# Kernel tuning notes

Hardware: AMD Instinct MI355X
Metric: run time of the kernel (lower is better)

Reference implementation:

```python
import jax, jax.numpy as jnp
import numpy as np

V, E, H, L, S, T = 100000, 256, 512, 50000, 512, 64


def setup_inputs() -> dict:
    key = jax.random.key(0)
    ks = jax.random.split(key, 14)
    s = 0.02
    return {
        "encoder_outputs": jax.random.normal(ks[0], (1, S, H), jnp.float32),
        "enc_h0": jax.random.normal(ks[1], (1, 1, H), jnp.float32),
        "enc_c0": jax.random.normal(ks[2], (1, 1, H), jnp.float32),
        "emb_table": jax.random.normal(ks[3], (V, E), jnp.float32) * s,
        "W_attn": jax.random.normal(ks[4], (H, E), jnp.float32) * s,
        "b_attn": jnp.zeros((H,), jnp.float32),
        "W_ih": jax.random.normal(ks[5], (4 * H, H), jnp.float32) * s,
        "W_hh": jax.random.normal(ks[6], (4 * H, H), jnp.float32) * s,
        "b_ih": jnp.zeros((4 * H,), jnp.float32),
        "b_hh": jnp.zeros((4 * H,), jnp.float32),
        "W_out": jax.random.normal(ks[7], (L, H), jnp.float32) * s,
        "b_out": jnp.zeros((L,), jnp.float32),
        "word_inputs": jax.random.randint(ks[8], (T,), 0, V),
        "labels": jax.random.randint(ks[9], (T,), 0, L),
    }


def reference(encoder_outputs, enc_h0, enc_c0, emb_table, W_attn, b_attn,
              W_ih, W_hh, b_ih, b_hh, W_out, b_out, word_inputs, labels):
    # batch == 1 throughout (matches forward_train); dropout is identity (eval).
    enc = encoder_outputs[0]          # [S, H]
    h0 = enc_h0[0, 0]                 # [H]  (bidirect hidden already flattened to 1x1xH)
    c0 = enc_c0[0, 0]                 # [H]

    def step(carry, xs):
        h, c = carry
        widx, label = xs
        e = emb_table[widx]                               # [E]   embedding lookup
        q = W_attn @ e + b_attn                           # [H]   attn projection (Linear)
        alphas = jax.nn.softmax(enc @ q)                  # [S]   bmm + softmax
        ctx = alphas @ enc                                # [H]   bmm -> context
        # single-step LSTM (PyTorch gate order: i, f, g, o)
        gates = W_ih @ ctx + b_ih + W_hh @ h + b_hh       # [4H]
        i, f, g, o = jnp.split(gates, 4)
        i = jax.nn.sigmoid(i); f = jax.nn.sigmoid(f)
        g = jnp.tanh(g);       o = jax.nn.sigmoid(o)
        c2 = f * c + i * g
        h2 = o * jnp.tanh(c2)
        logits = W_out @ h2 + b_out                       # [L]   hidden2tag
        ls = jax.nn.log_softmax(logits)
        # NLLLoss(ignore_index=0, reduction='sum')
        step_loss = jnp.where(label == 0, jnp.float32(0.0), -ls[label])
        return (h2, c2), step_loss

    (_, _), losses = jax.lax.scan(step, (h0, c0),
                                  (word_inputs, labels))
    return jnp.sum(losses)
```

## Files before the change

kernel.cpp:

```cpp
#include <hip/hip_runtime.h>
#include <hip/hip_bf16.h>

#define V_ 100000
#define E_ 256
#define H_ 512
#define L_ 50000
#define S_ 512
#define T_ 64
#define NB_ 782
#define NBP_ 784
#define NWG_ 32

typedef short bf16x8 __attribute__((ext_vector_type(8)));
typedef float f32x4 __attribute__((ext_vector_type(4)));

__device__ __forceinline__ float sigm(float x){ return 1.0f/(1.0f+__expf(-x)); }
__device__ __forceinline__ float tanh_fast(float x){
    x = fminf(fmaxf(x, -15.f), 15.f);
    float e = __expf(2.f * x);
    return __fdividef(e - 1.f, e + 1.f);
}
__device__ __forceinline__ unsigned bf16rne(float x){
    unsigned u = __float_as_uint(x);
    return (u + 0x7fffu + ((u >> 16) & 1u)) >> 16;
}
__device__ __forceinline__ float bcast(float v, int l){
    return __uint_as_float(__builtin_amdgcn_readlane(__float_as_uint(v), l));
}

__global__ __launch_bounds__(256) void k_attn(
    const float* __restrict__ enc, const float* __restrict__ emb,
    const float* __restrict__ W_attn, const float* __restrict__ b_attn,
    const int* __restrict__ word_inputs, float* __restrict__ ctx_out)
{
    __shared__ float e_l[E_];
    __shared__ float q_l[H_];
    __shared__ float sc[S_];
    __shared__ float red[8];
    const int t = blockIdx.x, tid = threadIdx.x;
    const int widx = word_inputs[t];

    e_l[tid] = emb[(long)widx * E_ + tid];
    __syncthreads();

    for (int rr = 0; rr < 2; ++rr) {
        int r = tid + rr * 256;
        const float4* wrow = (const float4*)(W_attn + r * E_);
        const float4* ev = (const float4*)e_l;
        float acc = b_attn[r];
        #pragma unroll 8
        for (int j = 0; j < E_ / 4; ++j) {
            float4 w = wrow[j], e4 = ev[j];
            acc += w.x*e4.x + w.y*e4.y + w.z*e4.z + w.w*e4.w;
        }
        q_l[r] = acc;
    }
    __syncthreads();

    for (int rr = 0; rr < 2; ++rr) {
        int s = tid + rr * 256;
        const float4* er = (const float4*)(enc + s * H_);
        const float4* qv = (const float4*)q_l;
        float acc = 0.f;
        #pragma unroll 8
        for (int j = 0; j < H_ / 4; ++j) {
            float4 a = er[j], b = qv[j];
            acc += a.x*b.x + a.y*b.y + a.z*b.z + a.w*b.w;
        }
        sc[s] = acc;
    }
    __syncthreads();

    float m = fmaxf(sc[tid], sc[tid + 256]);
    for (int off = 32; off; off >>= 1) m = fmaxf(m, __shfl_down(m, off));
    if ((tid & 63) == 0) red[tid >> 6] = m;
    __syncthreads();
    if (tid == 0) red[4] = fmaxf(fmaxf(red[0], red[1]), fmaxf(red[2], red[3]));
    __syncthreads();
    m = red[4];
    float e0 = __expf(sc[tid] - m), e1 = __expf(sc[tid + 256] - m);
    sc[tid] = e0; sc[tid + 256] = e1;
    float ssum = e0 + e1;
    for (int off = 32; off; off >>= 1) ssum += __shfl_down(ssum, off);
    if ((tid & 63) == 0) red[tid >> 6] = ssum;
    __syncthreads();
    if (tid == 0) red[5] = red[0] + red[1] + red[2] + red[3];
    __syncthreads();
    float inv = 1.0f / red[5];

    for (int rr = 0; rr < 2; ++rr) {
        int h = tid + rr * 256;
        float acc = 0.f;
        #pragma unroll 4
        for (int s = 0; s < S_; ++s) acc += sc[s] * enc[s * H_ + h];
        ctx_out[t * H_ + h] = acc * inv;
    }
}

__global__ __launch_bounds__(256) void k_gatepre(
    const float* __restrict__ ctx, const float* __restrict__ W_ih,
    const float* __restrict__ b_ih, const float* __restrict__ b_hh,
    float* __restrict__ A_pre)
{
    __shared__ float ctx_t[H_ * 65];
    __shared__ float w_l[8 * H_];
    const int tid = threadIdx.x;
    const int r0 = blockIdx.x * 8;

    for (int i = 0; i < 32; ++i) {
        int p = tid + i * 256;
        int t = p >> 7, k4 = p & 127;
        float4 v = ((const float4*)ctx)[p];
        ctx_t[(k4*4+0)*65 + t] = v.x;
        ctx_t[(k4*4+1)*65 + t] = v.y;
        ctx_t[(k4*4+2)*65 + t] = v.z;
        ctx_t[(k4*4+3)*65 + t] = v.w;
    }
    for (int i = 0; i < 4; ++i) {
        int p = tid + i * 256;
        int row = p >> 7, k4 = p & 127;
        float4 v = ((const float4*)W_ih)[(r0 + row) * (H_/4) + k4];
        float* dst = &w_l[row * H_ + k4 * 4];
        dst[0]=v.x; dst[1]=v.y; dst[2]=v.z; dst[3]=v.w;
    }
    __syncthreads();

    const int t = tid & 63, half = tid >> 6;
    const float* w0 = &w_l[(half*2+0) * H_];
    const float* w1 = &w_l[(half*2+1) * H_];
    float acc0 = 0.f, acc1 = 0.f;
    #pragma unroll 4
    for (int k = 0; k < H_; ++k) {
        float cv = ctx_t[k * 65 + t];
        acc0 += w0[k] * cv;
        acc1 += w1[k] * cv;
    }
    int ra = r0 + half * 2, rb = ra + 1;
    A_pre[t * 2048 + ra] = acc0 + b_ih[ra] + b_hh[ra];
    A_pre[t * 2048 + rb] = acc1 + b_ih[rb] + b_hh[rb];
}

__global__ __launch_bounds__(256, 1) void k_lstm(
    const float* __restrict__ W_hh, const float* __restrict__ A_pre,
    const float* __restrict__ h0, const float* __restrict__ c0,
    float* __restrict__ h_buf)
{
    __shared__ float A_l[T_ * 64];
    __shared__ float red[2][4][64];

    const int tid = threadIdx.x, w = blockIdx.x;
    const int base = w * 16;
    const int lane = tid & 63;
    const int ks   = tid >> 6;
    const int G = ((lane >> 4) << 9) + base + (lane & 15);

    float wr[128];
    {
        const float4* wsrc = (const float4*)(W_hh + (long)G * H_ + ks * 128);
        #pragma unroll
        for (int i = 0; i < 32; ++i) {
            float4 v = wsrc[i];
            wr[4*i+0]=v.x; wr[4*i+1]=v.y; wr[4*i+2]=v.z; wr[4*i+3]=v.w;
        }
    }
    #pragma unroll
    for (int i = 0; i < 128; ++i) asm volatile("" : "+v"(wr[i]));

    for (int i = 0; i < 16; ++i) {
        int p = tid + i * 256;
        int tt = p >> 6, rr = p & 63;
        A_l[p] = A_pre[tt * 2048 + ((rr >> 4) << 9) + base + (rr & 15)];
    }
    float c_reg = 0.f;
    if (tid < 16) c_reg = c0[base + tid];

    const unsigned SENT = 0xFFFFFFFFu;

    for (int t = 0; t < T_; ++t) {
        float vh0f, vh1f;
        if (t == 0) {
            vh0f = h0[ks * 128 + lane];
            vh1f = h0[ks * 128 + 64 + lane];
            __syncthreads();
        } else {
            const unsigned* hb = (const unsigned*)h_buf + (t - 1) * H_ + ks * 128;
            unsigned u0 = __hip_atomic_load(hb + lane, __ATOMIC_RELAXED,
                                            __HIP_MEMORY_SCOPE_AGENT);
            while (u0 == SENT) {
                __builtin_amdgcn_s_sleep(1);
                u0 = __hip_atomic_load(hb + lane, __ATOMIC_RELAXED,
                                       __HIP_MEMORY_SCOPE_AGENT);
            }
            unsigned u1 = __hip_atomic_load(hb + 64 + lane, __ATOMIC_RELAXED,
                                            __HIP_MEMORY_SCOPE_AGENT);
            while (u1 == SENT) {
                __builtin_amdgcn_s_sleep(1);
                u1 = __hip_atomic_load(hb + 64 + lane, __ATOMIC_RELAXED,
                                       __HIP_MEMORY_SCOPE_AGENT);
            }
            vh0f = __uint_as_float(u0);
            vh1f = __uint_as_float(u1);
        }

        float a0 = 0.f, a1 = 0.f, a2 = 0.f, a3 = 0.f;
        #pragma unroll
        for (int k = 0; k < 64; k += 4) {
            a0 += bcast(vh0f, k+0) * wr[k+0];
            a1 += bcast(vh0f, k+1) * wr[k+1];
            a2 += bcast(vh0f, k+2) * wr[k+2];
            a3 += bcast(vh0f, k+3) * wr[k+3];
        }
        #pragma unroll
        for (int k = 0; k < 64; k += 4) {
            a0 += bcast(vh1f, k+0) * wr[64+k+0];
            a1 += bcast(vh1f, k+1) * wr[64+k+1];
            a2 += bcast(vh1f, k+2) * wr[64+k+2];
            a3 += bcast(vh1f, k+3) * wr[64+k+3];
        }
        red[t & 1][ks][lane] = (a0 + a1) + (a2 + a3);
        __syncthreads();

        if (tid < 16) {
            float g4[4];
            #pragma unroll
            for (int g = 0; g < 4; ++g) {
                int r = g * 16 + lane;
                g4[g] = red[t & 1][0][r] + red[t & 1][1][r]
                      + red[t & 1][2][r] + red[t & 1][3][r]
                      + A_l[t * 64 + r];
            }
            float gi = sigm(g4[0]);
            float gf = sigm(g4[1]);
            float gg = tanh_fast(g4[2]);
            float go = sigm(g4[3]);
            float c2 = gf * c_reg + gi * gg;
            c_reg = c2;
            float h2 = go * tanh_fast(c2);
            __hip_atomic_store((unsigned*)h_buf + t * H_ + base + lane,
                               __float_as_uint(h2),
                               __ATOMIC_RELAXED, __HIP_MEMORY_SCOPE_AGENT);
        }
    }
}

__global__ __launch_bounds__(256) void k_out(
    const float* __restrict__ W_out, const float* __restrict__ b_out,
    const float* __restrict__ h_buf, const int* __restrict__ labels,
    float* __restrict__ pm, float* __restrict__ ps, float* __restrict__ ll)
{
    __shared__ __align__(16) unsigned char smem[65536];
    const int tid = threadIdx.x;
    const int r0 = blockIdx.x * 64;
    const int lane = tid & 63, w = tid >> 6;
    const int g = lane >> 4, li = lane & 15;

    for (int i = 0; i < 32; ++i) {
        int p = tid + i * 256;
        int t = p >> 7, k4 = p & 127;
        float4 v = ((const float4*)h_buf)[p];
        unsigned p01 = bf16rne(v.x) | (bf16rne(v.y) << 16);
        unsigned p23 = bf16rne(v.z) | (bf16rne(v.w) << 16);
        unsigned byte = (unsigned)(t * 1024 + k4 * 8) ^ ((unsigned)(t & 7) << 4);
        *(uint2*)(smem + byte) = make_uint2(p01, p23);
    }

    f32x4 acc0 = {0.f,0.f,0.f,0.f}, acc1 = {0.f,0.f,0.f,0.f};
    f32x4 acc2 = {0.f,0.f,0.f,0.f}, acc3 = {0.f,0.f,0.f,0.f};
    __syncthreads();

    int rrow = r0 + w * 16 + li;
    int rw = rrow < L_ ? rrow : (L_ - 1);
    const float* ap = W_out + (long)rw * H_ + g * 8;

    #pragma unroll
    for (int kk = 0; kk < 16; ++kk) {
        float4 va = *(const float4*)(ap + kk * 32);
        float4 vb = *(const float4*)(ap + kk * 32 + 4);
        union { unsigned u[4]; bf16x8 v; } A;
        A.u[0] = bf16rne(va.x) | (bf16rne(va.y) << 16);
        A.u[1] = bf16rne(va.z) | (bf16rne(va.w) << 16);
        A.u[2] = bf16rne(vb.x) | (bf16rne(vb.y) << 16);
        A.u[3] = bf16rne(vb.z) | (bf16rne(vb.w) << 16);

        #pragma unroll
        for (int nt = 0; nt < 4; ++nt) {
            int t = nt * 16 + li;
            unsigned byte = (unsigned)(t * 1024 + kk * 64 + g * 16)
                          ^ ((unsigned)(t & 7) << 4);
            bf16x8 B = *(const bf16x8*)(smem + byte);
            f32x4* accp = (nt == 0) ? &acc0 : (nt == 1) ? &acc1
                        : (nt == 2) ? &acc2 : &acc3;
            *accp = __builtin_amdgcn_mfma_f32_16x16x32_bf16(A.v, B, *accp, 0, 0, 0);
        }
    }
    __syncthreads();

    float* lg   = (float*)smem;
    float* redb = (float*)(smem + 64 * 65 * 4);
    float* gmax = redb + 256;

    #pragma unroll
    for (int nt = 0; nt < 4; ++nt) {
        const f32x4 a = (nt == 0) ? acc0 : (nt == 1) ? acc1
                      : (nt == 2) ? acc2 : acc3;
        int t = nt * 16 + li;
        #pragma unroll
        for (int q = 0; q < 4; ++q) {
            int rloc = w * 16 + g * 4 + q;
            int r = r0 + rloc;
            float v = -1e30f;
            if (r < L_) v = a[q] + b_out[r];
            lg[rloc * 65 + t] = v;
        }
    }
    __syncthreads();

    const int t = tid & 63, part = tid >> 6;
    float m = -1e30f;
    #pragma unroll
    for (int r16 = 0; r16 < 16; ++r16)
        m = fmaxf(m, lg[(part*16 + r16)*65 + t]);
    redb[part*64 + t] = m;
    __syncthreads();
    if (part == 0)
        gmax[t] = fmaxf(fmaxf(redb[t], redb[64+t]), fmaxf(redb[128+t], redb[192+t]));
    __syncthreads();
    float gm = gmax[t];
    float s = 0.f;
    #pragma unroll
    for (int r16 = 0; r16 < 16; ++r16)
        s += __expf(lg[(part*16 + r16)*65 + t] - gm);
    __syncthreads();
    redb[part*64 + t] = s;
    __syncthreads();
    if (part == 0) {
        pm[t * NBP_ + blockIdx.x] = gm;
        ps[t * NBP_ + blockIdx.x] = redb[t] + redb[64+t] + redb[128+t] + redb[192+t];
        int lb = labels[t];
        if (lb >= r0 && lb < r0 + 64) ll[t] = lg[(lb - r0)*65 + t];
    }
}

__global__ __launch_bounds__(256) void k_final(
    const float* __restrict__ pm, const float* __restrict__ ps,
    const float* __restrict__ ll, const int* __restrict__ labels,
    float* __restrict__ out)
{
    __shared__ float rbuf[8];
    const int t = blockIdx.x, tid = threadIdx.x;
    float m = -1e30f;
    for (int b = tid; b < NB_; b += 256) m = fmaxf(m, pm[t * NBP_ + b]);
    for (int off = 32; off; off >>= 1) m = fmaxf(m, __shfl_down(m, off));
    if ((tid & 63) == 0) rbuf[tid >> 6] = m;
    __syncthreads();
    if (tid == 0) rbuf[4] = fmaxf(fmaxf(rbuf[0], rbuf[1]), fmaxf(rbuf[2], rbuf[3]));
    __syncthreads();
    float M = rbuf[4];
    __syncthreads();
    float s = 0.f;
    for (int b = tid; b < NB_; b += 256)
        s += ps[t * NBP_ + b] * __expf(pm[t * NBP_ + b] - M);
    for (int off = 32; off; off >>= 1) s += __shfl_down(s, off);
    if ((tid & 63) == 0) rbuf[tid >> 6] = s;
    __syncthreads();
    if (tid == 0) {
        float S = rbuf[0] + rbuf[1] + rbuf[2] + rbuf[3];
        int lb = labels[t];
        if (lb != 0) {
            float loss = -(ll[t] - M - __logf(S));
            atomicAdd(out, loss);
        }
    }
}

extern "C" void kernel_launch(void* const* d_in, const int* in_sizes, int n_in,
                              void* d_out, int out_size, void* d_ws, size_t ws_size,
                              hipStream_t stream)
{
    (void)in_sizes; (void)n_in; (void)out_size; (void)ws_size;
    const float* enc    = (const float*)d_in[0];
    const float* h0     = (const float*)d_in[1];
    const float* c0     = (const float*)d_in[2];
    const float* emb    = (const float*)d_in[3];
    const float* W_attn = (const float*)d_in[4];
    const float* b_attn = (const float*)d_in[5];
    const float* W_ih   = (const float*)d_in[6];
    const float* W_hh   = (const float*)d_in[7];
    const float* b_ih   = (const float*)d_in[8];
    const float* b_hh   = (const float*)d_in[9];
    const float* W_out  = (const float*)d_in[10];
    const float* b_out  = (const float*)d_in[11];
    const int* widx     = (const int*)d_in[12];
    const int* labels   = (const int*)d_in[13];
    float* out = (float*)d_out;

    char* ws = (char*)d_ws;
    float* ctx   = (float*)(ws + 0);
    float* A_pre = (float*)(ws + 131072);
    float* h_buf = (float*)(ws + 655360);
    float* pm    = (float*)(ws + 786688);
    float* ps    = (float*)(ws + 987392);
    float* ll    = (float*)(ws + 1188096);

    hipMemsetAsync(h_buf, 0xFF, T_ * H_ * sizeof(float), stream);
    hipMemsetAsync(out, 0, sizeof(float), stream);

    k_attn<<<T_, 256, 0, stream>>>(enc, emb, W_attn, b_attn, widx, ctx);
    k_gatepre<<<256, 256, 0, stream>>>(ctx, W_ih, b_ih, b_hh, A_pre);
    k_lstm<<<NWG_, 256, 0, stream>>>(W_hh, A_pre, h0, c0, h_buf);
    k_out<<<NB_, 256, 0, stream>>>(W_out, b_out, h_buf, labels, pm, ps, ll);
    k_final<<<T_, 256, 0, stream>>>(pm, ps, ll, labels, out);
}
```

Before: 253.8 us.

## Widen LSTM blocks to 512 threads and prefetch W_out into L2 concurrently

The recurrent LSTM kernel now runs 512 threads per block, so each wave holds 64 weights instead of 128 and needs only one h load per step. The gate reduction moves from a single 16-lane group to a wave-wide shuffle. Extra blocks are launched alongside the 32 recurrent blocks; they stream all of W_out and discard the sum, meant to warm L2/LLC so the later output projection reads from cache while the latency-bound recurrence is running. The risks are that the 100MB W_out may not fit in cache, and that the prefetch traffic could slow the spin-waiting recurrent blocks.

```diff
diff --git a/kernel.cpp b/kernel.cpp
--- a/kernel.cpp
+++ b/kernel.cpp
@@ -10,6 +10,7 @@
 #define NB_ 782
 #define NBP_ 784
 #define NWG_ 32
+#define NPF_ 128
 
 typedef short bf16x8 __attribute__((ext_vector_type(8)));
 typedef float f32x4 __attribute__((ext_vector_type(4)));
@@ -140,105 +141,103 @@
     A_pre[t * 2048 + rb] = acc1 + b_ih[rb] + b_hh[rb];
 }
 
-__global__ __launch_bounds__(256, 1) void k_lstm(
+__global__ __launch_bounds__(512, 2) void k_lstm(
     const float* __restrict__ W_hh, const float* __restrict__ A_pre,
     const float* __restrict__ h0, const float* __restrict__ c0,
-    float* __restrict__ h_buf)
-{
+    float* __restrict__ h_buf, const float* __restrict__ W_out)
+{
+    const int tid = threadIdx.x, wg = blockIdx.x;
+
+    if (wg >= NWG_) {
+        const long total = (long)L_ * H_ / 4;
+        const long stride = (long)NPF_ * 512;
+        const float4* src = (const float4*)W_out;
+        float acc = 0.f;
+        for (long i = (long)(wg - NWG_) * 512 + tid; i < total; i += stride) {
+            float4 v = src[i];
+            acc += v.x + v.y + v.z + v.w;
+        }
+        asm volatile("" :: "v"(acc));
+        return;
+    }
+
     __shared__ float A_l[T_ * 64];
-    __shared__ float red[2][4][64];
-
-    const int tid = threadIdx.x, w = blockIdx.x;
-    const int base = w * 16;
+    __shared__ float red[2][8][64];
+
+    const int base = wg * 16;
     const int lane = tid & 63;
     const int ks   = tid >> 6;
     const int G = ((lane >> 4) << 9) + base + (lane & 15);
 
-    float wr[128];
+    float w[64];
     {
-        const float4* wsrc = (const float4*)(W_hh + (long)G * H_ + ks * 128);
+        const float4* wsrc = (const float4*)(W_hh + (long)G * H_ + ks * 64);
         #pragma unroll
-        for (int i = 0; i < 32; ++i) {
+        for (int i = 0; i < 16; ++i) {
             float4 v = wsrc[i];
-            wr[4*i+0]=v.x; wr[4*i+1]=v.y; wr[4*i+2]=v.z; wr[4*i+3]=v.w;
+            w[4*i+0]=v.x; w[4*i+1]=v.y; w[4*i+2]=v.z; w[4*i+3]=v.w;
         }
     }
     #pragma unroll
-    for (int i = 0; i < 128; ++i) asm volatile("" : "+v"(wr[i]));
-
-    for (int i = 0; i < 16; ++i) {
-        int p = tid + i * 256;
+    for (int i = 0; i < 64; ++i) asm volatile("" : "+v"(w[i]));
+
+    for (int i = 0; i < 8; ++i) {
+        int p = tid + i * 512;
         int tt = p >> 6, rr = p & 63;
         A_l[p] = A_pre[tt * 2048 + ((rr >> 4) << 9) + base + (rr & 15)];
     }
     float c_reg = 0.f;
     if (tid < 16) c_reg = c0[base + tid];
+    __syncthreads();
 
     const unsigned SENT = 0xFFFFFFFFu;
 
     for (int t = 0; t < T_; ++t) {
-        float vh0f, vh1f;
+        float hv;
         if (t == 0) {
-            vh0f = h0[ks * 128 + lane];
-            vh1f = h0[ks * 128 + 64 + lane];
-            __syncthreads();
+            hv = h0[ks * 64 + lane];
         } else {
-            const unsigned* hb = (const unsigned*)h_buf + (t - 1) * H_ + ks * 128;
-            unsigned u0 = __hip_atomic_load(hb + lane, __ATOMIC_RELAXED,
-                                            __HIP_MEMORY_SCOPE_AGENT);
-            while (u0 == SENT) {
+            const unsigned* hb = (const unsigned*)h_buf + (t - 1) * H_ + ks * 64;
+            unsigned u = __hip_atomic_load(hb + lane, __ATOMIC_RELAXED,
+                                           __HIP_MEMORY_SCOPE_AGENT);
+            while (u == SENT) {
                 __builtin_amdgcn_s_sleep(1);
-                u0 = __hip_atomic_load(hb + lane, __ATOMIC_RELAXED,
-                                       __HIP_MEMORY_SCOPE_AGENT);
+                u = __hip_atomic_load(hb + lane, __ATOMIC_RELAXED,
+                                      __HIP_MEMORY_SCOPE_AGENT);
             }
-            unsigned u1 = __hip_atomic_load(hb + 64 + lane, __ATOMIC_RELAXED,
-                                            __HIP_MEMORY_SCOPE_AGENT);
-            while (u1 == SENT) {
-                __builtin_amdgcn_s_sleep(1);
-                u1 = __hip_atomic_load(hb + 64 + lane, __ATOMIC_RELAXED,
-                                       __HIP_MEMORY_SCOPE_AGENT);
-            }
-            vh0f = __uint_as_float(u0);
-            vh1f = __uint_as_float(u1);
+            hv = __uint_as_float(u);
         }
 
         float a0 = 0.f, a1 = 0.f, a2 = 0.f, a3 = 0.f;
         #pragma unroll
-        for (int k = 0; k < 64; k += 4) {
-            a0 += bcast(vh0f, k+0) * wr[k+0];
-            a1 += bcast(vh0f, k+1) * wr[k+1];
-            a2 += bcast(vh0f, k+2) * wr[k+2];
-            a3 += bcast(vh0f, k+3) * wr[k+3];
-        }
-        #pragma unroll
-        for (int k = 0; k < 64; k += 4) {
-            a0 += bcast(vh1f, k+0) * wr[64+k+0];
-            a1 += bcast(vh1f, k+1) * wr[64+k+1];
-            a2 += bcast(vh1f, k+2) * wr[64+k+2];
-            a3 += bcast(vh1f, k+3) * wr[64+k+3];
+        for (int j = 0; j < 64; j += 4) {
+            a0 += bcast(hv, j+0) * w[j+0];
+            a1 += bcast(hv, j+1) * w[j+1];
+            a2 += bcast(hv, j+2) * w[j+2];
+            a3 += bcast(hv, j+3) * w[j+3];
         }
         red[t & 1][ks][lane] = (a0 + a1) + (a2 + a3);
         __syncthreads();
 
-        if (tid < 16) {
-            float g4[4];
+        if (ks == 0) {
+            float s = A_l[t * 64 + lane];
             #pragma unroll
-            for (int g = 0; g < 4; ++g) {
-                int r = g * 16 + lane;
-                g4[g] = red[t & 1][0][r] + red[t & 1][1][r]
-                      + red[t & 1][2][r] + red[t & 1][3][r]
-                      + A_l[t * 64 + r];
+            for (int k2 = 0; k2 < 8; ++k2) s += red[t & 1][k2][lane];
+            float gf_ = __shfl_down(s, 16);
+            float gg_ = __shfl_down(s, 32);
+            float go_ = __shfl_down(s, 48);
+            if (lane < 16) {
+                float gi = sigm(s);
+                float gf = sigm(gf_);
+                float gg = tanh_fast(gg_);
+                float go = sigm(go_);
+                float c2 = gf * c_reg + gi * gg;
+                c_reg = c2;
+                float h2 = go * tanh_fast(c2);
+                __hip_atomic_store((unsigned*)h_buf + t * H_ + base + lane,
+                                   __float_as_uint(h2),
+                                   __ATOMIC_RELAXED, __HIP_MEMORY_SCOPE_AGENT);
             }
-            float gi = sigm(g4[0]);
-            float gf = sigm(g4[1]);
-            float gg = tanh_fast(g4[2]);
-            float go = sigm(g4[3]);
-            float c2 = gf * c_reg + gi * gg;
-            c_reg = c2;
-            float h2 = go * tanh_fast(c2);
-            __hip_atomic_store((unsigned*)h_buf + t * H_ + base + lane,
-                               __float_as_uint(h2),
-                               __ATOMIC_RELAXED, __HIP_MEMORY_SCOPE_AGENT);
         }
     }
 }
@@ -407,7 +406,7 @@
 
     k_attn<<<T_, 256, 0, stream>>>(enc, emb, W_attn, b_attn, widx, ctx);
     k_gatepre<<<256, 256, 0, stream>>>(ctx, W_ih, b_ih, b_hh, A_pre);
-    k_lstm<<<NWG_, 256, 0, stream>>>(W_hh, A_pre, h0, c0, h_buf);
+    k_lstm<<<NWG_ + NPF_, 512, 0, stream>>>(W_hh, A_pre, h0, c0, h_buf, W_out);
     k_out<<<NB_, 256, 0, stream>>>(W_out, b_out, h_buf, labels, pm, ps, ll);
     k_final<<<T_, 256, 0, stream>>>(pm, ps, ll, labels, out);
 }
```

Result: faster. 237.1 us (-6.6%).
